# Kernel tuning notes

Hardware: AMD Instinct MI355X
Metric: run time of the kernel (lower is better)

The kernel has to match this reference:

```python
import jax, jax.numpy as jnp
import numpy as np
import math

SIZE = (60, 270, 480)           # full video T, H, W
CHANNELS = 14                   # sum of per-level grid channels 8+4+2
GRID_SIZES = [(60, 16, 16, 8), (30, 8, 8, 4), (15, 4, 4, 2)]
IDX_MAX = (60, 3, 5)            # patch grid -> patch_size (1, 90, 96)
PADDING = (0, 1, 1)
N_PATCH = 64
MANIP_LBASE = 2.0
MANIP_LEVELS = 8
INIT_SCALE = 1e-3


def setup_inputs() -> dict:
    key = jax.random.key(0)
    kt, kh, kw = jax.random.split(key, 3)
    idx = jnp.stack([
        jax.random.randint(kt, (N_PATCH,), 0, IDX_MAX[0]),
        jax.random.randint(kh, (N_PATCH,), 0, IDX_MAX[1]),
        jax.random.randint(kw, (N_PATCH,), 0, IDX_MAX[2]),
    ], axis=1).astype(jnp.int32)
    inp = {
        "idx": idx,
        "idx_max": jnp.asarray(IDX_MAX, dtype=jnp.int32),
        "padding": jnp.asarray(PADDING, dtype=jnp.int32),
    }
    for i, (T, H, W, C) in enumerate(GRID_SIZES):
        k = jax.random.fold_in(key, 10 + i)
        inp[f"grid{i}"] = jax.random.normal(k, (T * H * W, C), jnp.float32) * INIT_SCALE
    return inp


def _pixel_idx_1d(ix, size_d, nmax_d, pad_d):
    # ix: [N] patch index along one dim -> ([N, P+2*pad] clipped pixel idx, mask)
    p = size_d // nmax_d
    offs = jnp.arange(-pad_d, p + pad_d)
    raw = ix[:, None] * p + offs[None, :]
    mask = ((raw >= 0) & (raw < size_d)).astype(jnp.float32)
    return jnp.clip(raw, 0, size_d - 1), mask


def reference(idx, idx_max, padding, grid0, grid1, grid2):
    T, H, W = SIZE
    im = tuple(int(v) for v in np.asarray(idx_max))
    pad = tuple(int(v) for v in np.asarray(padding))
    patch = tuple(SIZE[d] // im[d] for d in range(3))
    ppad = tuple(patch[d] + 2 * pad[d] for d in range(3))

    # Multi-level grids -> trilinear upsample to full (T,H,W,C_i), concat on C.
    # jax.image.resize 'trilinear' uses half-pixel centers == torch align_corners=False.
    enc_splits = []
    for g, (Tg, Hg, Wg, Cg) in zip((grid0, grid1, grid2), GRID_SIZES):
        enc_splits.append(jax.image.resize(g.reshape(Tg, Hg, Wg, Cg), (T, H, W, Cg), method="trilinear"))
    enc = jnp.concatenate(enc_splits, axis=-1).reshape(T * H * W, CHANNELS)

    it, mt = _pixel_idx_1d(idx[:, 0], T, im[0], pad[0])
    ih, mh = _pixel_idx_1d(idx[:, 1], H, im[1], pad[1])
    iw, mw = _pixel_idx_1d(idx[:, 2], W, im[2], pad[2])

    flat = (it[:, :, None, None] * (H * W) + ih[:, None, :, None] * W + iw[:, None, None, :]).reshape(-1)
    mask = (mt[:, :, None, None] * mh[:, None, :, None] * mw[:, None, None, :]).reshape(-1, 1)

    t_embed = (mask * enc[flat]).reshape((idx.shape[0],) + ppad + (CHANNELS,))

    bases = (MANIP_LBASE ** jnp.arange(MANIP_LEVELS, dtype=jnp.float32)) * math.pi
    v = idx[:, 0].astype(jnp.float32)[:, None] * bases
    t_manip = jnp.concatenate([jnp.sin(v), jnp.cos(v)], axis=-1)  # [N, 2*levels]

    return t_embed, t_manip
```

## Files before the change

### kernel.cpp

```cpp
#include <hip/hip_runtime.h>
#include <math.h>


#define N_PATCH 64
#define PPAD_H 92
#define PPAD_W 98
#define CH 14
#define PIX_PER_PATCH (PPAD_H * PPAD_W)
#define PIX_PER_CHUNK 256
#define PIX_PER_BLOCK 512
#define BLOCKS_PER_PATCH ((PIX_PER_PATCH + PIX_PER_BLOCK - 1) / PIX_PER_BLOCK)
#define TOTAL_EMBED (N_PATCH * PIX_PER_PATCH * CH)
#define TOTAL_MANIP (N_PATCH * 16)

__device__ __forceinline__ float lerpf(float a, float b, float f) {
    return a + f * (b - a);
}

__global__ __launch_bounds__(256) void embed_kernel(
    const int* __restrict__ idx,
    const float* __restrict__ g0,
    const float* __restrict__ g1,
    const float* __restrict__ g2,
    float* __restrict__ out)
{
    __shared__ float s_g0[16 * 16 * 8];
    __shared__ float s_g1[8 * 8 * 4];
    __shared__ float s_g2[4 * 4 * 2];
    __shared__ int   s_ho0[3][PPAD_H];
    __shared__ int   s_ho1[3][PPAD_H];
    __shared__ float s_hf [3][PPAD_H];
    __shared__ int   s_wo0[3][PPAD_W];
    __shared__ int   s_wo1[3][PPAD_W];
    __shared__ float s_wf [3][PPAD_W];
    __shared__ float s_buf[PIX_PER_CHUNK * CH];

    const int tid = threadIdx.x;
    const int n   = blockIdx.y;
    const int it  = idx[3 * n + 0];
    const int ih  = idx[3 * n + 1];
    const int iw  = idx[3 * n + 2];

    {
        const float4* src = (const float4*)(g0 + (size_t)it * (16 * 16 * 8));
        float4* dst = (float4*)s_g0;
        for (int i = tid; i < 512; i += 256) dst[i] = src[i];
    }
    {
        float xt = ((float)it + 0.5f) * 0.5f - 0.5f;
        float ftf = floorf(xt);
        float ft  = xt - ftf;
        int t0 = (int)ftf;
        int t0c = min(max(t0, 0), 29), t1c = min(t0 + 1, 29);
        const float* p0 = g1 + t0c * (8 * 8 * 4);
        const float* p1 = g1 + t1c * (8 * 8 * 4);
        if (tid < 256) s_g1[tid] = lerpf(p0[tid], p1[tid], ft);
    }
    {
        float xt = ((float)it + 0.5f) * 0.25f - 0.5f;
        float ftf = floorf(xt);
        float ft  = xt - ftf;
        int t0 = (int)ftf;
        int t0c = min(max(t0, 0), 14), t1c = min(t0 + 1, 14);
        const float* p0 = g2 + t0c * (4 * 4 * 2);
        const float* p1 = g2 + t1c * (4 * 4 * 2);
        if (tid < 32) s_g2[tid] = lerpf(p0[tid], p1[tid], ft);
    }
    if (tid < PPAD_H) {
        int rh = ih * 90 + tid - 1;
        bool ok = (unsigned)rh < 270u;
        const int   Hgs[3] = {16, 8, 4};
        const int   rst[3] = {16 * 8, 8 * 4, 4 * 2};
        const float shs[3] = {(float)((double)16 / 270.0),
                              (float)((double)8  / 270.0),
                              (float)((double)4  / 270.0)};
        #pragma unroll
        for (int l = 0; l < 3; ++l) {
            float xh = ((float)rh + 0.5f) * shs[l] - 0.5f;
            float ff = floorf(xh);
            float f  = xh - ff;
            int h0 = (int)ff;
            int h0c = min(max(h0, 0), Hgs[l] - 1);
            int h1c = min(h0 + 1, Hgs[l] - 1);
            s_ho0[l][tid] = ok ? h0c * rst[l] : -1;
            s_ho1[l][tid] = h1c * rst[l];
            s_hf [l][tid] = f;
        }
    }
    if (tid < PPAD_W) {
        int rw = iw * 96 + tid - 1;
        bool ok = (unsigned)rw < 480u;
        const int   Wgs[3] = {16, 8, 4};
        const int   cst[3] = {8, 4, 2};
        const float sws[3] = {(float)((double)16 / 480.0),
                              (float)((double)8  / 480.0),
                              (float)((double)4  / 480.0)};
        #pragma unroll
        for (int l = 0; l < 3; ++l) {
            float xw = ((float)rw + 0.5f) * sws[l] - 0.5f;
            float ff = floorf(xw);
            float f  = xw - ff;
            int w0 = (int)ff;
            int w0c = min(max(w0, 0), Wgs[l] - 1);
            int w1c = min(w0 + 1, Wgs[l] - 1);
            s_wo0[l][tid] = ok ? w0c * cst[l] : -1;
            s_wo1[l][tid] = w1c * cst[l];
            s_wf [l][tid] = f;
        }
    }

    if (blockIdx.x == 0 && n == 0) {
        float* om = out + TOTAL_EMBED;
        for (int e = tid; e < TOTAL_MANIP; e += 256) {
            int nn = e >> 4;
            int j  = e & 15;
            int l  = j & 7;
            float base = (float)M_PI * (float)(1 << l);
            float v = (float)idx[3 * nn + 0] * base;
            double dv = (double)v;
            om[e] = (float)((j < 8) ? sin(dv) : cos(dv));
        }
    }
    __syncthreads();

    const int pstart = blockIdx.x * PIX_PER_BLOCK;
    const int pend   = min(pstart + PIX_PER_BLOCK, PIX_PER_PATCH);
    float* outp = out + (size_t)n * PIX_PER_PATCH * CH;

    for (int pbase = pstart; pbase < pend; pbase += PIX_PER_CHUNK) {
        const int cnt = min(PIX_PER_CHUNK, pend - pbase);
        const int p   = pbase + tid;

        if (tid < cnt) {
            int hh = p / PPAD_W;
            int ww = p - hh * PPAD_W;
            float2* b = (float2*)(s_buf + tid * CH);

            int ho0_0 = s_ho0[0][hh];
            int wo0_0 = s_wo0[0][ww];
            if ((ho0_0 | wo0_0) < 0) {
                float2 z = make_float2(0.f, 0.f);
                b[0] = z; b[1] = z; b[2] = z; b[3] = z; b[4] = z; b[5] = z; b[6] = z;
            } else {
                float res[CH];
                {
                    int ho1 = s_ho1[0][hh], wo1 = s_wo1[0][ww];
                    float fh = s_hf[0][hh], fw = s_wf[0][ww];
                    const float4* c00 = (const float4*)(s_g0 + ho0_0 + wo0_0);
                    const float4* c01 = (const float4*)(s_g0 + ho0_0 + wo1);
                    const float4* c10 = (const float4*)(s_g0 + ho1 + wo0_0);
                    const float4* c11 = (const float4*)(s_g0 + ho1 + wo1);
                    #pragma unroll
                    for (int q = 0; q < 2; ++q) {
                        float4 a = c00[q], bb = c01[q], c = c10[q], d = c11[q];
                        res[q * 4 + 0] = lerpf(lerpf(a.x, bb.x, fw), lerpf(c.x, d.x, fw), fh);
                        res[q * 4 + 1] = lerpf(lerpf(a.y, bb.y, fw), lerpf(c.y, d.y, fw), fh);
                        res[q * 4 + 2] = lerpf(lerpf(a.z, bb.z, fw), lerpf(c.z, d.z, fw), fh);
                        res[q * 4 + 3] = lerpf(lerpf(a.w, bb.w, fw), lerpf(c.w, d.w, fw), fh);
                    }
                }
                {
                    int ho0 = s_ho0[1][hh], ho1 = s_ho1[1][hh];
                    int wo0 = s_wo0[1][ww], wo1 = s_wo1[1][ww];
                    float fh = s_hf[1][hh], fw = s_wf[1][ww];
                    float4 a = *(const float4*)(s_g1 + ho0 + wo0);
                    float4 bb = *(const float4*)(s_g1 + ho0 + wo1);
                    float4 c = *(const float4*)(s_g1 + ho1 + wo0);
                    float4 d = *(const float4*)(s_g1 + ho1 + wo1);
                    res[8]  = lerpf(lerpf(a.x, bb.x, fw), lerpf(c.x, d.x, fw), fh);
                    res[9]  = lerpf(lerpf(a.y, bb.y, fw), lerpf(c.y, d.y, fw), fh);
                    res[10] = lerpf(lerpf(a.z, bb.z, fw), lerpf(c.z, d.z, fw), fh);
                    res[11] = lerpf(lerpf(a.w, bb.w, fw), lerpf(c.w, d.w, fw), fh);
                }
                {
                    int ho0 = s_ho0[2][hh], ho1 = s_ho1[2][hh];
                    int wo0 = s_wo0[2][ww], wo1 = s_wo1[2][ww];
                    float fh = s_hf[2][hh], fw = s_wf[2][ww];
                    float2 a = *(const float2*)(s_g2 + ho0 + wo0);
                    float2 bb = *(const float2*)(s_g2 + ho0 + wo1);
                    float2 c = *(const float2*)(s_g2 + ho1 + wo0);
                    float2 d = *(const float2*)(s_g2 + ho1 + wo1);
                    res[12] = lerpf(lerpf(a.x, bb.x, fw), lerpf(c.x, d.x, fw), fh);
                    res[13] = lerpf(lerpf(a.y, bb.y, fw), lerpf(c.y, d.y, fw), fh);
                }
                b[0] = make_float2(res[0],  res[1]);
                b[1] = make_float2(res[2],  res[3]);
                b[2] = make_float2(res[4],  res[5]);
                b[3] = make_float2(res[6],  res[7]);
                b[4] = make_float2(res[8],  res[9]);
                b[5] = make_float2(res[10], res[11]);
                b[6] = make_float2(res[12], res[13]);
            }
        }
        __syncthreads();

        const int nf4 = cnt * CH / 4;
        const float4* sb = (const float4*)s_buf;
        float4* gb = (float4*)(outp + (size_t)pbase * CH);
        for (int j = tid; j < nf4; j += 256) gb[j] = sb[j];
        __syncthreads();
    }
}

extern "C" void kernel_launch(void* const* d_in, const int* in_sizes, int n_in,
                              void* d_out, int out_size, void* d_ws, size_t ws_size,
                              hipStream_t stream) {
    const int*   idx = (const int*)  d_in[0];
    const float* g0  = (const float*)d_in[3];
    const float* g1  = (const float*)d_in[4];
    const float* g2  = (const float*)d_in[5];
    float* out = (float*)d_out;

    dim3 grid(BLOCKS_PER_PATCH, N_PATCH);
    embed_kernel<<<grid, 256, 0, stream>>>(idx, g0, g1, g2, out);
}
```

Baseline: 14.31 us.

## Compute one float2 output per thread directly, removing LDS staging buffer

```diff
diff --git a/kernel.cpp b/kernel.cpp
--- a/kernel.cpp
+++ b/kernel.cpp
@@ -7,11 +7,14 @@
 #define PPAD_W 98
 #define CH 14
 #define PIX_PER_PATCH (PPAD_H * PPAD_W)
-#define PIX_PER_CHUNK 256
-#define PIX_PER_BLOCK 512
-#define BLOCKS_PER_PATCH ((PIX_PER_PATCH + PIX_PER_BLOCK - 1) / PIX_PER_BLOCK)
+#define F2_PER_PATCH (PIX_PER_PATCH * CH / 2)
+#define BLOCKS_PER_PATCH 28
+#define SLICE (F2_PER_PATCH / BLOCKS_PER_PATCH)
 #define TOTAL_EMBED (N_PATCH * PIX_PER_PATCH * CH)
 #define TOTAL_MANIP (N_PATCH * 16)
+
+#define L1_BASE 2048
+#define L2_BASE 2304
 
 __device__ __forceinline__ float lerpf(float a, float b, float f) {
     return a + f * (b - a);
@@ -24,16 +27,9 @@
     const float* __restrict__ g2,
     float* __restrict__ out)
 {
-    __shared__ float s_g0[16 * 16 * 8];
-    __shared__ float s_g1[8 * 8 * 4];
-    __shared__ float s_g2[4 * 4 * 2];
-    __shared__ int   s_ho0[3][PPAD_H];
-    __shared__ int   s_ho1[3][PPAD_H];
-    __shared__ float s_hf [3][PPAD_H];
-    __shared__ int   s_wo0[3][PPAD_W];
-    __shared__ int   s_wo1[3][PPAD_W];
-    __shared__ float s_wf [3][PPAD_W];
-    __shared__ float s_buf[PIX_PER_CHUNK * CH];
+    __shared__ float  s_grid[2336];
+    __shared__ float4 s_hl[3][PPAD_H];
+    __shared__ float4 s_wl[3][PPAD_W];
 
     const int tid = threadIdx.x;
     const int n   = blockIdx.y;
@@ -42,8 +38,8 @@
     const int iw  = idx[3 * n + 2];
 
     {
-        const float4* src = (const float4*)(g0 + (size_t)it * (16 * 16 * 8));
-        float4* dst = (float4*)s_g0;
+        const float4* src = (const float4*)(g0 + (size_t)it * 2048);
+        float4* dst = (float4*)s_grid;
         for (int i = tid; i < 512; i += 256) dst[i] = src[i];
     }
     {
@@ -52,9 +48,9 @@
         float ft  = xt - ftf;
         int t0 = (int)ftf;
         int t0c = min(max(t0, 0), 29), t1c = min(t0 + 1, 29);
-        const float* p0 = g1 + t0c * (8 * 8 * 4);
-        const float* p1 = g1 + t1c * (8 * 8 * 4);
-        if (tid < 256) s_g1[tid] = lerpf(p0[tid], p1[tid], ft);
+        const float* p0 = g1 + t0c * 256;
+        const float* p1 = g1 + t1c * 256;
+        if (tid < 256) s_grid[L1_BASE + tid] = lerpf(p0[tid], p1[tid], ft);
     }
     {
         float xt = ((float)it + 0.5f) * 0.25f - 0.5f;
@@ -62,13 +58,13 @@
         float ft  = xt - ftf;
         int t0 = (int)ftf;
         int t0c = min(max(t0, 0), 14), t1c = min(t0 + 1, 14);
-        const float* p0 = g2 + t0c * (4 * 4 * 2);
-        const float* p1 = g2 + t1c * (4 * 4 * 2);
-        if (tid < 32) s_g2[tid] = lerpf(p0[tid], p1[tid], ft);
+        const float* p0 = g2 + t0c * 32;
+        const float* p1 = g2 + t1c * 32;
+        if (tid < 32) s_grid[L2_BASE + tid] = lerpf(p0[tid], p1[tid], ft);
     }
     if (tid < PPAD_H) {
         int rh = ih * 90 + tid - 1;
-        bool ok = (unsigned)rh < 270u;
+        float ok = ((unsigned)rh < 270u) ? 1.0f : 0.0f;
         const int   Hgs[3] = {16, 8, 4};
         const int   rst[3] = {16 * 8, 8 * 4, 4 * 2};
         const float shs[3] = {(float)((double)16 / 270.0),
@@ -82,14 +78,13 @@
             int h0 = (int)ff;
             int h0c = min(max(h0, 0), Hgs[l] - 1);
             int h1c = min(h0 + 1, Hgs[l] - 1);
-            s_ho0[l][tid] = ok ? h0c * rst[l] : -1;
-            s_ho1[l][tid] = h1c * rst[l];
-            s_hf [l][tid] = f;
+            s_hl[l][tid] = make_float4(__int_as_float(h0c * rst[l]),
+                                       __int_as_float(h1c * rst[l]), f, ok);
         }
     }
     if (tid < PPAD_W) {
         int rw = iw * 96 + tid - 1;
-        bool ok = (unsigned)rw < 480u;
+        float ok = ((unsigned)rw < 480u) ? 1.0f : 0.0f;
         const int   Wgs[3] = {16, 8, 4};
         const int   cst[3] = {8, 4, 2};
         const float sws[3] = {(float)((double)16 / 480.0),
@@ -103,9 +98,8 @@
             int w0 = (int)ff;
             int w0c = min(max(w0, 0), Wgs[l] - 1);
             int w1c = min(w0 + 1, Wgs[l] - 1);
-            s_wo0[l][tid] = ok ? w0c * cst[l] : -1;
-            s_wo1[l][tid] = w1c * cst[l];
-            s_wf [l][tid] = f;
+            s_wl[l][tid] = make_float4(__int_as_float(w0c * cst[l]),
+                                       __int_as_float(w1c * cst[l]), f, ok);
         }
     }
 
@@ -121,84 +115,41 @@
             om[e] = (float)((j < 8) ? sin(dv) : cos(dv));
         }
     }
+
     __syncthreads();
 
-    const int pstart = blockIdx.x * PIX_PER_BLOCK;
-    const int pend   = min(pstart + PIX_PER_BLOCK, PIX_PER_PATCH);
-    float* outp = out + (size_t)n * PIX_PER_PATCH * CH;
+    const int lj0 = blockIdx.x * SLICE;
+    const int ljend = lj0 + SLICE;
+    float2* o = ((float2*)out) + (size_t)n * F2_PER_PATCH;
 
-    for (int pbase = pstart; pbase < pend; pbase += PIX_PER_CHUNK) {
-        const int cnt = min(PIX_PER_CHUNK, pend - pbase);
-        const int p   = pbase + tid;
+    for (int lj = lj0 + tid; lj < ljend; lj += 256) {
+        unsigned p = (unsigned)lj / 7u;
+        int q = lj - 7 * (int)p;
+        unsigned hh = p / 98u;
+        int ww = (int)p - 98 * (int)hh;
 
-        if (tid < cnt) {
-            int hh = p / PPAD_W;
-            int ww = p - hh * PPAD_W;
-            float2* b = (float2*)(s_buf + tid * CH);
+        int lvl = (q >= 4) + (q >= 6);
+        int cb = 2 * q;
+        if (lvl == 1) cb = L1_BASE - 8 + 2 * q;
+        if (lvl == 2) cb = L2_BASE;
 
-            int ho0_0 = s_ho0[0][hh];
-            int wo0_0 = s_wo0[0][ww];
-            if ((ho0_0 | wo0_0) < 0) {
-                float2 z = make_float2(0.f, 0.f);
-                b[0] = z; b[1] = z; b[2] = z; b[3] = z; b[4] = z; b[5] = z; b[6] = z;
-            } else {
-                float res[CH];
-                {
-                    int ho1 = s_ho1[0][hh], wo1 = s_wo1[0][ww];
-                    float fh = s_hf[0][hh], fw = s_wf[0][ww];
-                    const float4* c00 = (const float4*)(s_g0 + ho0_0 + wo0_0);
-                    const float4* c01 = (const float4*)(s_g0 + ho0_0 + wo1);
-                    const float4* c10 = (const float4*)(s_g0 + ho1 + wo0_0);
-                    const float4* c11 = (const float4*)(s_g0 + ho1 + wo1);
-                    #pragma unroll
-                    for (int q = 0; q < 2; ++q) {
-                        float4 a = c00[q], bb = c01[q], c = c10[q], d = c11[q];
-                        res[q * 4 + 0] = lerpf(lerpf(a.x, bb.x, fw), lerpf(c.x, d.x, fw), fh);
-                        res[q * 4 + 1] = lerpf(lerpf(a.y, bb.y, fw), lerpf(c.y, d.y, fw), fh);
-                        res[q * 4 + 2] = lerpf(lerpf(a.z, bb.z, fw), lerpf(c.z, d.z, fw), fh);
-                        res[q * 4 + 3] = lerpf(lerpf(a.w, bb.w, fw), lerpf(c.w, d.w, fw), fh);
-                    }
-                }
-                {
-                    int ho0 = s_ho0[1][hh], ho1 = s_ho1[1][hh];
-                    int wo0 = s_wo0[1][ww], wo1 = s_wo1[1][ww];
-                    float fh = s_hf[1][hh], fw = s_wf[1][ww];
-                    float4 a = *(const float4*)(s_g1 + ho0 + wo0);
-                    float4 bb = *(const float4*)(s_g1 + ho0 + wo1);
-                    float4 c = *(const float4*)(s_g1 + ho1 + wo0);
-                    float4 d = *(const float4*)(s_g1 + ho1 + wo1);
-                    res[8]  = lerpf(lerpf(a.x, bb.x, fw), lerpf(c.x, d.x, fw), fh);
-                    res[9]  = lerpf(lerpf(a.y, bb.y, fw), lerpf(c.y, d.y, fw), fh);
-                    res[10] = lerpf(lerpf(a.z, bb.z, fw), lerpf(c.z, d.z, fw), fh);
-                    res[11] = lerpf(lerpf(a.w, bb.w, fw), lerpf(c.w, d.w, fw), fh);
-                }
-                {
-                    int ho0 = s_ho0[2][hh], ho1 = s_ho1[2][hh];
-                    int wo0 = s_wo0[2][ww], wo1 = s_wo1[2][ww];
-                    float fh = s_hf[2][hh], fw = s_wf[2][ww];
-                    float2 a = *(const float2*)(s_g2 + ho0 + wo0);
-                    float2 bb = *(const float2*)(s_g2 + ho0 + wo1);
-                    float2 c = *(const float2*)(s_g2 + ho1 + wo0);
-                    float2 d = *(const float2*)(s_g2 + ho1 + wo1);
-                    res[12] = lerpf(lerpf(a.x, bb.x, fw), lerpf(c.x, d.x, fw), fh);
-                    res[13] = lerpf(lerpf(a.y, bb.y, fw), lerpf(c.y, d.y, fw), fh);
-                }
-                b[0] = make_float2(res[0],  res[1]);
-                b[1] = make_float2(res[2],  res[3]);
-                b[2] = make_float2(res[4],  res[5]);
-                b[3] = make_float2(res[6],  res[7]);
-                b[4] = make_float2(res[8],  res[9]);
-                b[5] = make_float2(res[10], res[11]);
-                b[6] = make_float2(res[12], res[13]);
-            }
-        }
-        __syncthreads();
+        float4 hl = s_hl[lvl][hh];
+        float4 wl = s_wl[lvl][ww];
+        int ho0 = __float_as_int(hl.x), ho1 = __float_as_int(hl.y);
+        int wo0 = __float_as_int(wl.x), wo1 = __float_as_int(wl.y);
+        float fh = hl.z, fw = wl.z;
+        float mm = hl.w * wl.w;
 
-        const int nf4 = cnt * CH / 4;
-        const float4* sb = (const float4*)s_buf;
-        float4* gb = (float4*)(outp + (size_t)pbase * CH);
-        for (int j = tid; j < nf4; j += 256) gb[j] = sb[j];
-        __syncthreads();
+        const float* gb = s_grid + cb;
+        float2 a = *(const float2*)(gb + ho0 + wo0);
+        float2 b = *(const float2*)(gb + ho0 + wo1);
+        float2 c = *(const float2*)(gb + ho1 + wo0);
+        float2 d = *(const float2*)(gb + ho1 + wo1);
+
+        float2 r;
+        r.x = mm * lerpf(lerpf(a.x, b.x, fw), lerpf(c.x, d.x, fw), fh);
+        r.y = mm * lerpf(lerpf(a.y, b.y, fw), lerpf(c.y, d.y, fw), fh);
+        o[lj] = r;
     }
 }
 
```

Result: slower. 15.53 us (+8.6%).
